# Kernel optimization log

Measured on AMD Instinct MI355X. Metric: run time of the kernel, lower is better.

The kernel has to match this reference:

```python
import jax, jax.numpy as jnp
import numpy as np

B, S, Ng, Np = 64, 128, 4096, 512

def setup_inputs() -> dict:
    key = jax.random.key(0)
    k = jax.random.split(key, 6)
    v = jax.random.normal(k[0], (B, S, 2), dtype=jnp.float32)
    p0 = jax.random.normal(k[1], (B, Np), dtype=jnp.float32)
    # Parameters (no biases anywhere, matching bias=False in the module)
    W_init = jax.random.normal(k[2], (Ng, Np), dtype=jnp.float32) / np.sqrt(Np)   # init_position_encoder
    W_ih = jax.random.normal(k[3], (Ng, 2), dtype=jnp.float32) / np.sqrt(Ng)      # RNN.weight_ih_l0
    W_hh = jax.random.normal(k[4], (Ng, Ng), dtype=jnp.float32) / np.sqrt(Ng)     # RNN.weight_hh_l0
    W_dec = jax.random.normal(k[5], (Np, Ng), dtype=jnp.float32) / np.sqrt(Ng)    # decoder
    return {"v": v, "p0": p0, "W_init": W_init, "W_ih": W_ih, "W_hh": W_hh, "W_dec": W_dec}

def reference(v, p0, W_init, W_ih, W_hh, W_dec):
    # h0 = Linear(Np -> Ng, no bias)(p0)
    h0 = p0 @ W_init.T                     # (B, Ng)
    # Precompute the tiny input projection for all timesteps at once
    vx = jnp.einsum('bsi,gi->sbg', v, W_ih)  # (S, B, Ng)
    def step(h, x_t):
        h = jax.nn.relu(x_t + h @ W_hh.T)  # h_t = relu(W_ih v_t + W_hh h_{t-1})
        return h, h
    _, hs = jax.lax.scan(step, h0, vx)      # hs: (S, B, Ng)
    g = jnp.transpose(hs, (1, 0, 2))        # (B, S, Ng), batch_first like torch RNN
    place_preds = g @ W_dec.T               # (B, S, Np)
    return place_preds
```

## Files before the change

kernel.cpp:

```cpp
#include <hip/hip_runtime.h>

typedef __attribute__((ext_vector_type(8))) short short8;
typedef __attribute__((ext_vector_type(4))) float f32x4;
union U16x8 { uint4 u4; short8 s8; };

__device__ inline float bf2f(unsigned short u){
  unsigned int x = ((unsigned int)u) << 16;
  float f; __builtin_memcpy(&f, &x, 4); return f;
}
__device__ inline unsigned short f2bf(float f){
  unsigned int x; __builtin_memcpy(&x, &f, 4);
  x = x + 0x7FFFu + ((x >> 16) & 1u);
  return (unsigned short)(x >> 16);
}
__device__ inline void split4(float4 f, uint2& hi, uint2& lo){
  unsigned short h0=f2bf(f.x), h1=f2bf(f.y), h2=f2bf(f.z), h3=f2bf(f.w);
  unsigned short l0=f2bf(f.x-bf2f(h0)), l1=f2bf(f.y-bf2f(h1)),
                 l2=f2bf(f.z-bf2f(h2)), l3=f2bf(f.w-bf2f(h3));
  hi = (uint2){(unsigned)h0 | ((unsigned)h1<<16), (unsigned)h2 | ((unsigned)h3<<16)};
  lo = (uint2){(unsigned)l0 | ((unsigned)l1<<16), (unsigned)l2 | ((unsigned)l3<<16)};
}
__device__ inline void split8(float4 f0, float4 f1, uint4& hi, uint4& lo){
  uint2 h0,l0,h1,l1; split4(f0,h0,l0); split4(f1,h1,l1);
  hi = (uint4){h0.x,h0.y,h1.x,h1.y};
  lo = (uint4){l0.x,l0.y,l1.x,l1.y};
}

#define MFMA16(a,b,c) __builtin_amdgcn_mfma_f32_16x16x32_bf16((a).s8,(b).s8,(c),0,0,0)

__device__ inline void st_f32_sc(float* p, float v){
  __hip_atomic_store(p, v, __ATOMIC_RELAXED, __HIP_MEMORY_SCOPE_AGENT);
}
__device__ inline void st_u32_sc(unsigned int* p, unsigned int v){
  __hip_atomic_store(p, v, __ATOMIC_RELAXED, __HIP_MEMORY_SCOPE_AGENT);
}
__device__ inline unsigned long long ld_u64_sc(const unsigned long long* p){
  return __hip_atomic_load(p, __ATOMIC_RELAXED, __HIP_MEMORY_SCOPE_AGENT);
}
__device__ inline uint4 ld_b128_sc(const unsigned short* p){
  uint4 r;
  asm volatile("global_load_dwordx4 %0, %1, off sc0 sc1"
               : "=&v"(r) : "v"(p) : "memory");
  return r;
}
__device__ inline unsigned int poll_flag(const unsigned int* p){
  unsigned int r;
  asm volatile("global_load_dword %0, %1, off sc0 sc1\n\ts_waitcnt vmcnt(0)"
               : "=&v"(r) : "v"(p) : "memory");
  return r;
}
__device__ inline void wait_vm0(){ asm volatile("s_waitcnt vmcnt(0)" ::: "memory"); }

__global__ __launch_bounds__(256)
void split_fp32(const float* __restrict__ x,
                unsigned short* __restrict__ hi,
                unsigned short* __restrict__ lo, int n4){
  int i = blockIdx.x * 256 + threadIdx.x;
  if (i >= n4) return;
  float4 v = ((const float4*)x)[i];
  ushort4 h, l;
  h.x = f2bf(v.x); l.x = f2bf(v.x - bf2f(h.x));
  h.y = f2bf(v.y); l.y = f2bf(v.y - bf2f(h.y));
  h.z = f2bf(v.z); l.z = f2bf(v.z - bf2f(h.z));
  h.w = f2bf(v.w); l.w = f2bf(v.w - bf2f(h.w));
  ((ushort4*)hi)[i] = h;
  ((ushort4*)lo)[i] = l;
}

__global__ __launch_bounds__(512, 2)
void h0_mm(const float* __restrict__ p0,
           const float* __restrict__ Wini,
           unsigned short* __restrict__ oHi,
           unsigned short* __restrict__ oLo)
{
  const int nb = blockIdx.x;
  const int tid = threadIdx.x, lane = tid & 63, wave = tid >> 6;
  const int quad = lane >> 4, l16 = lane & 15;
  const int mw = wave & 3, nw = wave >> 2;
  __shared__ __attribute__((aligned(16))) unsigned short BH[128*40];
  __shared__ __attribute__((aligned(16))) unsigned short BL[128*40];
  const int srow = tid >> 2, sk = (tid & 3) << 3;
  const float* wp = Wini + (size_t)(nb*128 + srow)*512 + sk;
  const float* ap = p0 + (size_t)(mw*16 + l16)*512 + quad*8;
  f32x4 acc[4];
  #pragma unroll
  for (int tn = 0; tn < 4; ++tn) acc[tn] = (f32x4){0.f,0.f,0.f,0.f};
  for (int kc = 0; kc < 16; ++kc){
    float4 f0 = *(const float4*)(wp + kc*32);
    float4 f1 = *(const float4*)(wp + kc*32 + 4);
    uint4 hi, lo; split8(f0, f1, hi, lo);
    __syncthreads();
    *(uint4*)&BH[srow*40 + sk] = hi;
    *(uint4*)&BL[srow*40 + sk] = lo;
    __syncthreads();
    float4 a0 = *(const float4*)(ap + kc*32);
    float4 a1 = *(const float4*)(ap + kc*32 + 4);
    uint4 ahi, alo; split8(a0, a1, ahi, alo);
    U16x8 aU, lU; aU.u4 = ahi; lU.u4 = alo;
    #pragma unroll
    for (int tn = 0; tn < 4; ++tn){
      U16x8 bh, bl;
      const int off = (nw*64 + tn*16 + l16)*40 + quad*8;
      bh.u4 = *(const uint4*)&BH[off];
      bl.u4 = *(const uint4*)&BL[off];
      acc[tn] = MFMA16(aU, bh, acc[tn]);
      acc[tn] = MFMA16(aU, bl, acc[tn]);
      acc[tn] = MFMA16(lU, bh, acc[tn]);
    }
  }
  #pragma unroll
  for (int tn = 0; tn < 4; ++tn){
    const int n = nb*128 + nw*64 + tn*16 + l16;
    #pragma unroll
    for (int r = 0; r < 4; ++r){
      const int row = mw*16 + quad*4 + r;
      const int g = n >> 3, gp = (g & ~7) | ((g & 7) ^ (row & 7));
      const int np = (gp << 3) | (n & 7);
      float val = acc[tn][r];
      unsigned short hh = f2bf(val);
      oHi[(size_t)row*4096 + np] = hh;
      oLo[(size_t)row*4096 + np] = f2bf(val - bf2f(hh));
    }
  }
}

__global__ __launch_bounds__(512, 2)
void rnn_persist(const float* __restrict__ W,
                 const float* __restrict__ v,
                 const float* __restrict__ Wih,
                 unsigned short* __restrict__ hHiA,
                 unsigned short* __restrict__ hLoA,
                 unsigned short* __restrict__ hHiB,
                 unsigned short* __restrict__ hLoB,
                 float* __restrict__ part,
                 unsigned int* __restrict__ bar,
                 unsigned short* __restrict__ G)
{
  const int bx = blockIdx.x, kb = bx & 7, nb = bx >> 3;
  const int tid = threadIdx.x, lane = tid & 63, wave = tid >> 6;
  const int quad = lane >> 4, l16 = lane & 15;
  __shared__ __attribute__((aligned(16))) unsigned short AH[32*512];
  __shared__ __attribute__((aligned(16))) unsigned short AL[32*512];

  unsigned int* pA       = bar;
  unsigned int* pB       = bar + 1024;
  unsigned int* prodDone = bar + 2048;

  uint4 whi[16], wlo[16];
  {
    const float* wp = W + (size_t)(nb*128 + wave*16 + l16)*4096 + kb*512 + quad*8;
    #pragma unroll
    for (int c = 0; c < 16; ++c){
      float4 f0 = *(const float4*)(wp + c*32);
      float4 f1 = *(const float4*)(wp + c*32 + 4);
      split8(f0, f1, whi[c], wlo[c]);
    }
  }

  const int redM = bx >> 2;
  const int nbase = ((bx & 3) << 10) + (tid << 1);
  const int cR = kb >> 1;
  const bool aRed = (bx < 128);
  const float4 wi = *(const float4*)(Wih + (size_t)nbase*2);

  for (int s = 0; s < 128; ++s){
    const unsigned short* hH = (s & 1) ? hHiB : hHiA;
    const unsigned short* hL = (s & 1) ? hLoB : hLoA;
    unsigned short* nHi = (s & 1) ? hHiA : hHiB;
    unsigned short* nLo = (s & 1) ? hLoA : hLoB;
    float* pbuf = part + (size_t)(s & 1) * 2097152;

    if (s > 0){
      if (tid < 32){
        const unsigned int* f = prodDone + (tid*4 + cR)*4;
        while ((int)poll_flag(f) < s) __builtin_amdgcn_s_sleep(1);
      }
      __syncthreads();
    }

    {
      uint4 stg[8];
      #pragma unroll
      for (int i = 0; i < 4; ++i){
        const int flat = tid + i*512, row = flat >> 6, g = flat & 63;
        stg[i]     = ld_b128_sc(hH + (size_t)row*4096 + (kb << 9) + g*8);
        stg[4 + i] = ld_b128_sc(hL + (size_t)row*4096 + (kb << 9) + g*8);
      }
      wait_vm0();
      #pragma unroll
      for (int i = 0; i < 4; ++i){
        const int flat = tid + i*512, row = flat >> 6, g = flat & 63;
        *(uint4*)&AH[row*512 + g*8] = stg[i];
        *(uint4*)&AL[row*512 + g*8] = stg[4 + i];
      }
    }
    __syncthreads();

    if (s > 0){
      if (tid >= 32 && tid < 64){
        const unsigned int* f = prodDone + (tid*4 + cR)*4;
        while ((int)poll_flag(f) < s) __builtin_amdgcn_s_sleep(1);
      }
      __syncthreads();
    }

    uint4 stgB[8];
    #pragma unroll
    for (int i = 0; i < 4; ++i){
      const int flat = tid + i*512, row = 32 + (flat >> 6), g = flat & 63;
      stgB[i]     = ld_b128_sc(hH + (size_t)row*4096 + (kb << 9) + g*8);
      stgB[4 + i] = ld_b128_sc(hL + (size_t)row*4096 + (kb << 9) + g*8);
    }

    {
      f32x4 a0[2], a1[2], a2[2];
      #pragma unroll
      for (int mt = 0; mt < 2; ++mt){
        a0[mt] = (f32x4){0.f,0.f,0.f,0.f};
        a1[mt] = (f32x4){0.f,0.f,0.f,0.f};
        a2[mt] = (f32x4){0.f,0.f,0.f,0.f};
      }
      #pragma unroll
      for (int c = 0; c < 16; ++c){
        U16x8 bh, bl; bh.u4 = whi[c]; bl.u4 = wlo[c];
        #pragma unroll
        for (int mt = 0; mt < 2; ++mt){
          const int row = mt*16 + l16;
          const int gk = c*4 + quad;
          const int phys = (gk & 56) | ((gk & 7) ^ (row & 7));
          U16x8 ah, al;
          ah.u4 = *(const uint4*)&AH[row*512 + phys*8];
          al.u4 = *(const uint4*)&AL[row*512 + phys*8];
          a0[mt] = MFMA16(ah, bh, a0[mt]);
          a1[mt] = MFMA16(ah, bl, a1[mt]);
          a2[mt] = MFMA16(al, bh, a2[mt]);
        }
      }
      float* pb = pbuf + (size_t)bx*8192 + wave*1024 + l16;
      #pragma unroll
      for (int mt = 0; mt < 2; ++mt)
        #pragma unroll
        for (int r = 0; r < 4; ++r)
          st_f32_sc(pb + (mt*16 + quad*4 + r)*16, a0[mt][r] + a1[mt][r] + a2[mt][r]);
    }
    wait_vm0();
    __syncthreads();
    if (tid == 0) st_u32_sc(&pA[bx*4], (unsigned)(s + 1));

    #pragma unroll
    for (int i = 0; i < 4; ++i){
      const int flat = tid + i*512, row = flat >> 6, g = flat & 63;
      *(uint4*)&AH[row*512 + g*8] = stgB[i];
      *(uint4*)&AL[row*512 + g*8] = stgB[4 + i];
    }
    __syncthreads();

    {
      f32x4 a0[2], a1[2], a2[2];
      #pragma unroll
      for (int mt = 0; mt < 2; ++mt){
        a0[mt] = (f32x4){0.f,0.f,0.f,0.f};
        a1[mt] = (f32x4){0.f,0.f,0.f,0.f};
        a2[mt] = (f32x4){0.f,0.f,0.f,0.f};
      }
      #pragma unroll
      for (int c = 0; c < 16; ++c){
        U16x8 bh, bl; bh.u4 = whi[c]; bl.u4 = wlo[c];
        #pragma unroll
        for (int mt = 0; mt < 2; ++mt){
          const int row = mt*16 + l16;
          const int gk = c*4 + quad;
          const int phys = (gk & 56) | ((gk & 7) ^ (row & 7));
          U16x8 ah, al;
          ah.u4 = *(const uint4*)&AH[row*512 + phys*8];
          al.u4 = *(const uint4*)&AL[row*512 + phys*8];
          a0[mt] = MFMA16(ah, bh, a0[mt]);
          a1[mt] = MFMA16(ah, bl, a1[mt]);
          a2[mt] = MFMA16(al, bh, a2[mt]);
        }
      }
      float* pb = pbuf + (size_t)bx*8192 + wave*1024 + l16;
      #pragma unroll
      for (int mt = 0; mt < 2; ++mt)
        #pragma unroll
        for (int r = 0; r < 4; ++r)
          st_f32_sc(pb + (32 + mt*16 + quad*4 + r)*16, a0[mt][r] + a1[mt][r] + a2[mt][r]);
    }
    wait_vm0();
    __syncthreads();
    if (tid == 0) st_u32_sc(&pB[bx*4], (unsigned)(s + 1));

    if (tid < 64){
      const unsigned int* f = (aRed ? pA : pB) + ((bx & 3)*64 + tid)*4;
      while ((int)poll_flag(f) < s + 1) __builtin_amdgcn_s_sleep(1);
    }
    __syncthreads();

    {
      float2 sum = {0.f, 0.f};
      const size_t off = (size_t)((nbase >> 4) & 7)*1024 + redM*16 + (nbase & 15);
      #pragma unroll
      for (int k2 = 0; k2 < 8; ++k2){
        unsigned long long q = ld_u64_sc((const unsigned long long*)
            (pbuf + (size_t)((nbase >> 7)*8 + k2)*8192 + off));
        float2 p; __builtin_memcpy(&p, &q, 8);
        sum.x += p.x; sum.y += p.y;
      }
      const float2 vv = *(const float2*)(v + ((size_t)redM*128 + s)*2);
      float v0 = fmaxf(sum.x + vv.x*wi.x + vv.y*wi.y, 0.f);
      float v1 = fmaxf(sum.y + vv.x*wi.z + vv.y*wi.w, 0.f);
      const unsigned short h0 = f2bf(v0), h1 = f2bf(v1);
      const unsigned short q0 = f2bf(v0 - bf2f(h0)), q1 = f2bf(v1 - bf2f(h1));
      const int g = nbase >> 3, gp = (g & ~7) | ((g & 7) ^ (redM & 7));
      const int np = (gp << 3) | (nbase & 7);
      st_u32_sc((unsigned int*)(nHi + (size_t)redM*4096 + np),
                (unsigned)h0 | ((unsigned)h1 << 16));
      st_u32_sc((unsigned int*)(nLo + (size_t)redM*4096 + np),
                (unsigned)q0 | ((unsigned)q1 << 16));
      wait_vm0();
      __builtin_nontemporal_store((unsigned)h0 | ((unsigned)h1 << 16),
          (unsigned int*)(G + (size_t)s*262144 + (size_t)redM*4096 + nbase));
    }
    __syncthreads();
    if (tid == 0) st_u32_sc(&prodDone[bx*4], (unsigned)(s + 1));
  }
}

__global__ __launch_bounds__(256, 1)
void decode_g(const unsigned short* __restrict__ G,
              const unsigned short* __restrict__ WdH,
              const unsigned short* __restrict__ WdL,
              float* __restrict__ out)
{
  const int tid = threadIdx.x, lane = tid & 63, wave = tid >> 6;
  const int quad = lane >> 4, l16 = lane & 15;
  const int wm = wave & 1, wn = wave >> 1;
  const int m0 = blockIdx.x * 128;
  const int n0 = blockIdx.y * 128;
  __shared__ __attribute__((aligned(16))) unsigned short BH[2][128*64];
  __shared__ __attribute__((aligned(16))) unsigned short BL[2][128*64];

  const unsigned short* gp[4];
  #pragma unroll
  for (int tm = 0; tm < 4; ++tm)
    gp[tm] = G + (size_t)(m0 + wm*64 + tm*16 + l16)*4096 + quad*8;

  #define LD_B(c, h4, l4) { _Pragma("unroll") \
    for (int i = 0; i < 4; ++i){ const int q = tid + i*256, row = q >> 3, gk = q & 7; \
      const size_t so = (size_t)(n0 + row)*4096 + (size_t)(c)*64 + gk*8; \
      (h4)[i] = *(const uint4*)(WdH + so); (l4)[i] = *(const uint4*)(WdL + so); } }
  #define ST_B(buf, h4, l4) { _Pragma("unroll") \
    for (int i = 0; i < 4; ++i){ const int q = tid + i*256, row = q >> 3, gk = q & 7; \
      const int phys = gk ^ (row & 7); \
      *(uint4*)&BH[buf][row*64 + phys*8] = (h4)[i]; \
      *(uint4*)&BL[buf][row*64 + phys*8] = (l4)[i]; } }
  #define LD_A(c, dst) { _Pragma("unroll") \
    for (int tm = 0; tm < 4; ++tm){ _Pragma("unroll") \
      for (int ks = 0; ks < 2; ++ks) \
        (dst)[tm][ks] = *(const uint4*)(gp[tm] + (size_t)(c)*64 + ks*32); } }

  f32x4 acc[4][4];
  #pragma unroll
  for (int a = 0; a < 4; ++a)
    #pragma unroll
    for (int b = 0; b < 4; ++b) acc[a][b] = (f32x4){0.f,0.f,0.f,0.f};

  uint4 pbh[4], pbl[4];
  uint4 ar[2][4][2];
  LD_B(0, pbh, pbl); ST_B(0, pbh, pbl);
  LD_A(0, ar[0]);
  LD_A(1, ar[1]);
  LD_B(1, pbh, pbl);
  __syncthreads();

  for (int c = 0; c < 64; ++c){
    const int cur = c & 1;
    #pragma unroll
    for (int ks = 0; ks < 2; ++ks){
      U16x8 bh[4], bl[4];
      #pragma unroll
      for (int tn = 0; tn < 4; ++tn){
        const int row = wn*64 + tn*16 + l16;
        const int gk = ks*4 + quad;
        const int phys = gk ^ (row & 7);
        bh[tn].u4 = *(const uint4*)&BH[cur][row*64 + phys*8];
        bl[tn].u4 = *(const uint4*)&BL[cur][row*64 + phys*8];
      }
      #pragma unroll
      for (int tm = 0; tm < 4; ++tm){
        U16x8 a; a.u4 = ar[cur][tm][ks];
        #pragma unroll
        for (int tn = 0; tn < 4; ++tn){
          acc[tm][tn] = MFMA16(a, bh[tn], acc[tm][tn]);
          acc[tm][tn] = MFMA16(a, bl[tn], acc[tm][tn]);
        }
      }
    }
    if (c + 2 < 64) LD_A(c+2, ar[cur]);
    if (c + 1 < 64){
      ST_B(cur ^ 1, pbh, pbl);
      if (c + 2 < 64) LD_B(c+2, pbh, pbl);
      __syncthreads();
    }
  }
  #pragma unroll
  for (int tm = 0; tm < 4; ++tm){
    #pragma unroll
    for (int tn = 0; tn < 4; ++tn){
      const int p = n0 + wn*64 + tn*16 + l16;
      #pragma unroll
      for (int r = 0; r < 4; ++r){
        const int rm = m0 + wm*64 + tm*16 + quad*4 + r;
        out[((size_t)(rm & 63)*128 + (rm >> 6))*512 + p] = acc[tm][tn][r];
      }
    }
  }
}

extern "C" void kernel_launch(void* const* d_in, const int* in_sizes, int n_in,
                              void* d_out, int out_size, void* d_ws, size_t ws_size,
                              hipStream_t stream) {
  const float* v    = (const float*)d_in[0];
  const float* p0   = (const float*)d_in[1];
  const float* Wini = (const float*)d_in[2];
  const float* Wih  = (const float*)d_in[3];
  const float* Whh  = (const float*)d_in[4];
  const float* Wdec = (const float*)d_in[5];
  float* out = (float*)d_out;
  char* wsb = (char*)d_ws;

  unsigned int*   bar  = (unsigned int*)(wsb + 0);
  unsigned short* hHiA = (unsigned short*)(wsb + 16384);
  unsigned short* hLoA = (unsigned short*)(wsb + 540672);
  unsigned short* hHiB = (unsigned short*)(wsb + 1064960);
  unsigned short* hLoB = (unsigned short*)(wsb + 1589248);
  float*          part = (float*)(wsb + 2113536);
  unsigned short* WdH  = (unsigned short*)(wsb + 18890752);
  unsigned short* WdL  = (unsigned short*)(wsb + 23085056);
  unsigned short* G    = (unsigned short*)(wsb + 27279360);

  hipMemsetAsync(bar, 0, 16384, stream);
  split_fp32<<<dim3(2048), dim3(256), 0, stream>>>(Wdec, WdH, WdL, 524288);
  h0_mm<<<dim3(32), dim3(512), 0, stream>>>(p0, Wini, hHiA, hLoA);
  rnn_persist<<<dim3(256), dim3(512), 0, stream>>>(Whh, v, Wih,
                                                   hHiA, hLoA, hHiB, hLoB,
                                                   part, bar, G);
  decode_g<<<dim3(64, 4), dim3(256), 0, stream>>>(G, WdH, WdL, out);
}
```

Baseline: 2.532 ms.

## Localize reduction to column-block groups and overlap first-half reduce with second-half MFMA

Reassigns the split-K reduction so each block reduces partials only from the 8 blocks sharing its column tile (nb), rather than from 64 blocks across the grid. Blocks with kb<4 reduce the rows 0-31 half right after its partials are published, before computing the second half. Blocks with kb>=4 reduce the rows 32-63 half at the end. Consumer waits now poll 16 producer flags instead of 32. This cuts the fan-in of inter-block flag dependencies and overlaps reduction with MFMA work, shortening the per-timestep critical path of the recurrent loop, at the cost of a more intricate cross-block ordering that must stay deadlock-free.

```diff
diff --git a/kernel.cpp b/kernel.cpp
--- a/kernel.cpp
+++ b/kernel.cpp
@@ -157,11 +157,11 @@
     }
   }
 
-  const int redM = bx >> 2;
-  const int nbase = ((bx & 3) << 10) + (tid << 1);
-  const int cR = kb >> 1;
-  const bool aRed = (bx < 128);
-  const float4 wi = *(const float4*)(Wih + (size_t)nbase*2);
+  const bool aRed = (kb < 4);
+  const int row_red = kb*8 + (tid >> 6);
+  const int c2 = (tid & 63) << 1;
+  const int gcol = nb*128 + c2;
+  const float4 wi = *(const float4*)(Wih + (size_t)gcol*2);
 
   for (int s = 0; s < 128; ++s){
     const unsigned short* hH = (s & 1) ? hHiB : hHiA;
@@ -171,8 +171,9 @@
     float* pbuf = part + (size_t)(s & 1) * 2097152;
 
     if (s > 0){
-      if (tid < 32){
-        const unsigned int* f = prodDone + (tid*4 + cR)*4;
+      if (tid < 16){
+        const int bxp = (4*kb + (tid >> 2))*8 + (tid & 3);
+        const unsigned int* f = prodDone + bxp*4;
         while ((int)poll_flag(f) < s) __builtin_amdgcn_s_sleep(1);
       }
       __syncthreads();
@@ -197,8 +198,9 @@
     __syncthreads();
 
     if (s > 0){
-      if (tid >= 32 && tid < 64){
-        const unsigned int* f = prodDone + (tid*4 + cR)*4;
+      if (tid < 16){
+        const int bxp = (4*kb + (tid >> 2))*8 + 4 + (tid & 3);
+        const unsigned int* f = prodDone + bxp*4;
         while ((int)poll_flag(f) < s) __builtin_amdgcn_s_sleep(1);
       }
       __syncthreads();
@@ -255,6 +257,41 @@
     }
     __syncthreads();
 
+    if (aRed){
+      if (tid < 8){
+        const unsigned int* f = pA + (nb*8 + tid)*4;
+        while ((int)poll_flag(f) < s + 1) __builtin_amdgcn_s_sleep(1);
+      }
+      __syncthreads();
+      {
+        const float* base = pbuf + (size_t)(c2 >> 4)*1024 + row_red*16 + (c2 & 15);
+        float2 sum = {0.f, 0.f};
+        #pragma unroll
+        for (int j = 0; j < 8; ++j){
+          unsigned long long q = ld_u64_sc((const unsigned long long*)
+              (base + (size_t)(nb*8 + j)*8192));
+          float2 p; __builtin_memcpy(&p, &q, 8);
+          sum.x += p.x; sum.y += p.y;
+        }
+        const float2 vv = *(const float2*)(v + ((size_t)row_red*128 + s)*2);
+        float v0 = fmaxf(sum.x + vv.x*wi.x + vv.y*wi.y, 0.f);
+        float v1 = fmaxf(sum.y + vv.x*wi.z + vv.y*wi.w, 0.f);
+        const unsigned short h0 = f2bf(v0), h1 = f2bf(v1);
+        const unsigned short q0 = f2bf(v0 - bf2f(h0)), q1 = f2bf(v1 - bf2f(h1));
+        const int g = gcol >> 3, gp = (g & ~7) | ((g & 7) ^ (row_red & 7));
+        const int np = (gp << 3) | (gcol & 7);
+        st_u32_sc((unsigned int*)(nHi + (size_t)row_red*4096 + np),
+                  (unsigned)h0 | ((unsigned)h1 << 16));
+        st_u32_sc((unsigned int*)(nLo + (size_t)row_red*4096 + np),
+                  (unsigned)q0 | ((unsigned)q1 << 16));
+        wait_vm0();
+        __builtin_nontemporal_store((unsigned)h0 | ((unsigned)h1 << 16),
+            (unsigned int*)(G + (size_t)s*262144 + (size_t)row_red*4096 + gcol));
+      }
+      __syncthreads();
+      if (tid == 0) st_u32_sc(&prodDone[bx*4], (unsigned)(s + 1));
+    }
+
     {
       f32x4 a0[2], a1[2], a2[2];
       #pragma unroll
@@ -290,39 +327,40 @@
     __syncthreads();
     if (tid == 0) st_u32_sc(&pB[bx*4], (unsigned)(s + 1));
 
-    if (tid < 64){
-      const unsigned int* f = (aRed ? pA : pB) + ((bx & 3)*64 + tid)*4;
-      while ((int)poll_flag(f) < s + 1) __builtin_amdgcn_s_sleep(1);
-    }
-    __syncthreads();
-
-    {
-      float2 sum = {0.f, 0.f};
-      const size_t off = (size_t)((nbase >> 4) & 7)*1024 + redM*16 + (nbase & 15);
-      #pragma unroll
-      for (int k2 = 0; k2 < 8; ++k2){
-        unsigned long long q = ld_u64_sc((const unsigned long long*)
-            (pbuf + (size_t)((nbase >> 7)*8 + k2)*8192 + off));
-        float2 p; __builtin_memcpy(&p, &q, 8);
-        sum.x += p.x; sum.y += p.y;
-      }
-      const float2 vv = *(const float2*)(v + ((size_t)redM*128 + s)*2);
-      float v0 = fmaxf(sum.x + vv.x*wi.x + vv.y*wi.y, 0.f);
-      float v1 = fmaxf(sum.y + vv.x*wi.z + vv.y*wi.w, 0.f);
-      const unsigned short h0 = f2bf(v0), h1 = f2bf(v1);
-      const unsigned short q0 = f2bf(v0 - bf2f(h0)), q1 = f2bf(v1 - bf2f(h1));
-      const int g = nbase >> 3, gp = (g & ~7) | ((g & 7) ^ (redM & 7));
-      const int np = (gp << 3) | (nbase & 7);
-      st_u32_sc((unsigned int*)(nHi + (size_t)redM*4096 + np),
-                (unsigned)h0 | ((unsigned)h1 << 16));
-      st_u32_sc((unsigned int*)(nLo + (size_t)redM*4096 + np),
-                (unsigned)q0 | ((unsigned)q1 << 16));
-      wait_vm0();
-      __builtin_nontemporal_store((unsigned)h0 | ((unsigned)h1 << 16),
-          (unsigned int*)(G + (size_t)s*262144 + (size_t)redM*4096 + nbase));
-    }
-    __syncthreads();
-    if (tid == 0) st_u32_sc(&prodDone[bx*4], (unsigned)(s + 1));
+    if (!aRed){
+      if (tid < 8){
+        const unsigned int* f = pB + (nb*8 + tid)*4;
+        while ((int)poll_flag(f) < s + 1) __builtin_amdgcn_s_sleep(1);
+      }
+      __syncthreads();
+      {
+        const float* base = pbuf + (size_t)(c2 >> 4)*1024 + row_red*16 + (c2 & 15);
+        float2 sum = {0.f, 0.f};
+        #pragma unroll
+        for (int j = 0; j < 8; ++j){
+          unsigned long long q = ld_u64_sc((const unsigned long long*)
+              (base + (size_t)(nb*8 + j)*8192));
+          float2 p; __builtin_memcpy(&p, &q, 8);
+          sum.x += p.x; sum.y += p.y;
+        }
+        const float2 vv = *(const float2*)(v + ((size_t)row_red*128 + s)*2);
+        float v0 = fmaxf(sum.x + vv.x*wi.x + vv.y*wi.y, 0.f);
+        float v1 = fmaxf(sum.y + vv.x*wi.z + vv.y*wi.w, 0.f);
+        const unsigned short h0 = f2bf(v0), h1 = f2bf(v1);
+        const unsigned short q0 = f2bf(v0 - bf2f(h0)), q1 = f2bf(v1 - bf2f(h1));
+        const int g = gcol >> 3, gp = (g & ~7) | ((g & 7) ^ (row_red & 7));
+        const int np = (gp << 3) | (gcol & 7);
+        st_u32_sc((unsigned int*)(nHi + (size_t)row_red*4096 + np),
+                  (unsigned)h0 | ((unsigned)h1 << 16));
+        st_u32_sc((unsigned int*)(nLo + (size_t)row_red*4096 + np),
+                  (unsigned)q0 | ((unsigned)q1 << 16));
+        wait_vm0();
+        __builtin_nontemporal_store((unsigned)h0 | ((unsigned)h1 << 16),
+            (unsigned int*)(G + (size_t)s*262144 + (size_t)row_red*4096 + gcol));
+      }
+      __syncthreads();
+      if (tid == 0) st_u32_sc(&prodDone[bx*4], (unsigned)(s + 1));
+    }
   }
 }
 
```

Result: faster. 2.461 ms (-2.8%).
